# Performance work log

Hardware: AMD Instinct MI355X
Metric: run time of the kernel (lower is better)

## Reference

```python
import jax, jax.numpy as jnp
import numpy as np

# dims: S slots, B batch, D pred-rep dim, E slot-embedding dim, H hidden/output dim, V per-slot vocab
S, B, D, E, H, V = 7, 4096, 1024, 128, 512, 200
D0 = D + E  # layer-0 LSTM input size


def setup_inputs() -> dict:
    key = jax.random.key(0)
    ks = jax.random.split(key, 12)
    rn = lambda k, shape, s=0.02: jax.random.normal(k, shape, jnp.float32) * s
    return {
        "pred_reps": jax.random.normal(ks[0], (B, D), jnp.float32),
        "slot_labels": jax.random.randint(ks[1], (S, B), 0, V),
        "emb": rn(ks[2], (S, V, E), 1.0),
        # layer 0: per-slot LSTMCell + highway params
        "Wih0": rn(ks[3], (S, 4 * H, D0)), "Whh0": rn(ks[4], (S, 4 * H, H)),
        "bih0": jnp.zeros((S, 4 * H), jnp.float32), "bhh0": jnp.zeros((S, 4 * H), jnp.float32),
        "hwW0": rn(ks[5], (S, H, D0 + H)), "hwb0": jnp.zeros((S, H), jnp.float32),
        "linW0": rn(ks[6], (S, H, D0)),
        # layer 1 (input size = H)
        "Wih1": rn(ks[7], (S, 4 * H, H)), "Whh1": rn(ks[8], (S, 4 * H, H)),
        "bih1": jnp.zeros((S, 4 * H), jnp.float32), "bhh1": jnp.zeros((S, 4 * H), jnp.float32),
        "hwW1": rn(ks[9], (S, H, 2 * H)), "hwb1": jnp.zeros((S, H), jnp.float32),
        "linW1": rn(ks[10], (S, H, H)),
    }


def _lstm_cell(x, h, c, Wih, Whh, bih, bhh):
    # torch LSTMCell: gates ordered i, f, g, o
    gates = x @ Wih.T + bih + h @ Whh.T + bhh
    i, f, g, o = jnp.split(gates, 4, axis=-1)
    c_new = jax.nn.sigmoid(f) * c + jax.nn.sigmoid(i) * jnp.tanh(g)
    h_new = jax.nn.sigmoid(o) * jnp.tanh(c_new)
    return h_new, c_new


def reference(pred_reps, slot_labels, emb, Wih0, Whh0, bih0, bhh0, hwW0, hwb0, linW0,
              Wih1, Whh1, bih1, bhh1, hwW1, hwb1, linW1):
    def step(carry, xs):
        h0, c0, h1, c1 = carry
        (tbl, idx, wih0, whh0, bi0, bh0, hw0, hb0, lw0,
         wih1, whh1, bi1, bh1, hw1, hb1, lw1) = xs
        # per-slot embedding gather + concat with predicate reps  -> [B, D0]
        x = jnp.concatenate([pred_reps, tbl[idx]], axis=-1)
        # layer 0 cell + highway gate
        h0n, c0n = _lstm_cell(x, h0, c0, wih0, whh0, bi0, bh0)
        gate0 = jax.nn.sigmoid(jnp.concatenate([x, h0n], axis=-1) @ hw0.T + hb0)
        x1 = gate0 * h0n + (1.0 - gate0) * (x @ lw0.T)
        # layer 1 cell (its highway output is dead code in the original: curr_input
        # after the last layer is discarded, so we skip it -- same math)
        h1n, c1n = _lstm_cell(x1, h1, c1, wih1, whh1, bi1, bh1)
        return (h0n, c0n, h1n, c1n), None

    init = tuple(jnp.zeros((B, H), pred_reps.dtype) for _ in range(4))
    xs = (emb, slot_labels, Wih0, Whh0, bih0, bhh0, hwW0, hwb0, linW0,
          Wih1, Whh1, bih1, bhh1, hwW1, hwb1, linW1)
    carry, _ = jax.lax.scan(step, init, xs)
    return carry[2]  # last_h: top-layer hidden after final slot
```

## Files before the change

kernel.cpp:

```cpp
#include <hip/hip_runtime.h>
#include <stdint.h>

typedef unsigned short u16;

#define S_   7
#define B_   4096
#define D_   1024
#define E_   128
#define H_   512
#define V_   200
#define D0_  1152
#define K0_  1664
#define KX1  1024
#define G4H  2048
#define XW   2048
#define X1W  2048

typedef __bf16 bf16x8 __attribute__((ext_vector_type(8)));
typedef float  f32x4  __attribute__((ext_vector_type(4)));
typedef u16    u16x8  __attribute__((ext_vector_type(8)));

__device__ __forceinline__ u16 f2bf(float f) {
  union { float f; uint32_t u; } v; v.f = f;
  uint32_t r = v.u + 0x7fffu + ((v.u >> 16) & 1u);
  return (u16)(r >> 16);
}
__device__ __forceinline__ float bf2f(u16 b) {
  union { uint32_t u; float f; } v; v.u = ((uint32_t)b) << 16;
  return v.f;
}
__device__ __forceinline__ float sigmoidf_(float x) { return 1.0f / (1.0f + __expf(-x)); }
__device__ __forceinline__ float tanhf_(float x) {
  float t = __expf(-2.f * fabsf(x));
  return copysignf((1.f - t) / (1.f + t), x);
}

__device__ __forceinline__ void glds16(const u16* g, u16* l) {
  __builtin_amdgcn_global_load_lds(
      (const __attribute__((address_space(1))) uint32_t*)g,
      (__attribute__((address_space(3))) uint32_t*)l, 16, 0, 0);
}

__device__ __forceinline__ void cvt8s(const float* src, u16* dst) {
  const float4* p = (const float4*)src;
  float4 x = p[0], y = p[1];
  u16x8 o;
  o[0]=f2bf(x.x); o[1]=f2bf(x.y); o[2]=f2bf(x.z); o[3]=f2bf(x.w);
  o[4]=f2bf(y.x); o[5]=f2bf(y.y); o[6]=f2bf(y.z); o[7]=f2bf(y.w);
  *(u16x8*)dst = o;
}

template<int KK, int P1, int P2, int KA, int KB>
__global__ void pack_gw4(const float* __restrict__ Wih, const float* __restrict__ Whh,
                         u16* __restrict__ dst) {
  const int NG = KK / 8;
  const int stride = gridDim.x * 256;
  int idx = blockIdx.x * 256 + threadIdx.x;
  #pragma unroll
  for (int u = 0; u < 4; ++u) {
    int i = idx + u * stride;
    int sr = i / NG, kg = i - sr * NG;
    int k8 = kg * 8;
    long s = sr >> 11;
    int  r = sr & 2047;
    int  g = r >> 9, j = r & 511;
    long drow = (s << 11) + ((j >> 4) * 64 + g * 16 + (j & 15));
    const float* sp = (k8 < P1) ? Wih + (long)sr * KA + k8
                    : (k8 < P2) ? Whh + (long)sr * KB + (k8 - P1)
                                : Wih + (long)sr * KA + P1 + (k8 - P2);
    cvt8s(sp, &dst[drow * KK + k8]);
  }
}

template<int KS, bool Z2>
__global__ void pack_hw4(const float* __restrict__ src, u16* __restrict__ dst, int off16) {
  const int NG = K0_ / 8;
  const int stride = gridDim.x * 256;
  int idx = blockIdx.x * 256 + threadIdx.x;
  #pragma unroll
  for (int u = 0; u < 4; ++u) {
    int i = idx + u * stride;
    int sj = i / NG, kg = i - sj * NG;
    int k8 = kg * 8;
    long s = sj >> 9;
    int  j = sj & 511;
    long drow = (s << 10) + ((j >> 4) * 32 + off16 + (j & 15));
    u16* d = &dst[drow * K0_ + k8];
    if (Z2 && k8 >= 1024 && k8 < 1536) {
      u16x8 z = {};
      *(u16x8*)d = z;
    } else {
      const float* sp = (k8 < 1024) ? src + (long)sj * KS + k8
                      : (k8 < 1536) ? src + (long)sj * KS + 1152 + (k8 - 1024)
                                    : src + (long)sj * KS + 1024 + (k8 - 1536);
      cvt8s(sp, d);
    }
  }
}

__global__ void pack_predz4(const float* __restrict__ pred, u16* __restrict__ dst) {
  const int NG = XW / 8;
  const int stride = gridDim.x * 256;
  int idx = blockIdx.x * 256 + threadIdx.x;
  #pragma unroll
  for (int u = 0; u < 4; ++u) {
    int i = idx + u * stride;
    int row = i / NG, kg = i - row * NG;
    int k8 = kg * 8;
    u16* d = &dst[(long)row * XW + k8];
    if (k8 < 1024) {
      cvt8s(pred + (long)row * D_ + k8, d);
    } else {
      u16x8 z = {};
      *(u16x8*)d = z;
    }
  }
}

__global__ void xgather(const float* __restrict__ emb, const int* __restrict__ labels,
                        u16* __restrict__ EMB) {
  int b = blockIdx.x;
  int e = threadIdx.x;
  #pragma unroll
  for (int s = 0; s < S_; ++s) {
    int ix = labels[s * B_ + b];
    EMB[((long)(s * B_ + b)) * E_ + e] = f2bf(emb[((long)(s * V_ + ix)) * E_ + e]);
  }
}

__global__ void bias_sum(const float* __restrict__ a, const float* __restrict__ b,
                         float* __restrict__ o, int n) {
  int i = blockIdx.x * 256 + threadIdx.x;
  if (i < n) o[i] = a[i] + b[i];
}
__global__ void zero_f(float* __restrict__ p, int n) {
  for (int i = blockIdx.x * 256 + threadIdx.x; i < n; i += gridDim.x * 256) p[i] = 0.f;
}
__global__ void zero_u16k(u16* __restrict__ p, int n) {
  for (int i = blockIdx.x * 256 + threadIdx.x; i < n; i += gridDim.x * 256) p[i] = 0;
}

struct GemmP {
  const u16* r0; const u16* r1; const u16* r2;
  const u16* W;
  const float* bsum;
  float* cbuf;
  u16* hdst;
  float* hf32;
  const u16* h0src;
  int ld0, ld1, ld2, t1, t2, ldw, nt, ntn, cpx, hld, hoff, h0ld, mode;
};

__global__ __launch_bounds__(256)
void gemm_multi(GemmP pa, GemmP pb, GemmP pc, int nA, int nAB) {
  __shared__ __align__(16) u16 lds[4 * 8192];
  const int b = blockIdx.x;
  GemmP P = pc; int base = nAB;
  if (b < nAB) { P = pb; base = nA; }
  if (b < nA)  { P = pa; base = 0; }
  const int bidx = b - base;

  u16* lA = lds;
  u16* lW = lds + 2 * 8192;
  const int tid  = threadIdx.x;
  const int lane = tid & 63;
  const int wave = tid >> 6;
  const int bid  = (bidx & 7) * P.cpx + (bidx >> 3);
  const int tn = bid % P.ntn;
  const int tm = bid / P.ntn;
  const long row0 = (long)tm * 128;
  const long col0 = (long)tn * 128;
  const int wm = (wave >> 1) * 64;
  const int wn = (wave & 1) * 64;
  const int fr = lane & 15;
  const int fk = (lane >> 4) * 8;
  const int wr = wave * 32;

  const int srow = wr + (lane >> 3);
  const int scol = ((lane & 7) ^ ((lane >> 3) & 7)) * 8;
  const u16* gr0 = P.r0 + (row0 + srow) * (long)P.ld0 + scol;
  const u16* gr1 = P.r1 + (row0 + srow) * (long)P.ld1 + scol;
  const u16* gr2 = P.r2 + (row0 + srow) * (long)P.ld2 + scol;
  const u16* gw  = P.W  + (col0 + srow) * (long)P.ldw + scol;
  const int dst0 = wr * 64 + lane * 8;

  auto stage = [&](int t, int buf) {
    const u16* g; long ld;
    if (t < P.t1)      { g = gr0 + (long)t * 64;            ld = P.ld0; }
    else if (t < P.t2) { g = gr1 + (long)(t - P.t1) * 64;   ld = P.ld1; }
    else               { g = gr2 + (long)(t - P.t2) * 64;   ld = P.ld2; }
    const u16* gww = gw + (long)t * 64;
    u16* dA = lA + buf * 8192 + dst0;
    u16* dW = lW + buf * 8192 + dst0;
    #pragma unroll
    for (int i = 0; i < 4; ++i) {
      glds16(g   + (long)(i * 8) * ld,    dA + i * 512);
      glds16(gww + (long)(i * 8) * P.ldw, dW + i * 512);
    }
  };

  int aoff[4], woff[4];
  #pragma unroll
  for (int m = 0; m < 4; ++m) aoff[m] = (wm + m * 16 + fr) * 64;
  #pragma unroll
  for (int n = 0; n < 4; ++n) woff[n] = (wn + n * 16 + fr) * 64;
  const int swz = (fr & 7) << 3;
  const int kk0 = (0 + fk) ^ swz;
  const int kk1 = (32 + fk) ^ swz;

  f32x4 acc[4][4] = {};
  const int nt = P.nt;

  stage(0, 0);

  for (int t = 0; t < nt; ++t) {
    __syncthreads();
    if (t + 1 < nt) stage(t + 1, (t + 1) & 1);
    const u16* Ab = lA + (t & 1) * 8192;
    const u16* Wb = lW + (t & 1) * 8192;
    bf16x8 af0[4], wf0[4], af1[4], wf1[4];
    #pragma unroll
    for (int m = 0; m < 4; ++m) af0[m] = *(const bf16x8*)&Ab[aoff[m] + kk0];
    #pragma unroll
    for (int n = 0; n < 4; ++n) wf0[n] = *(const bf16x8*)&Wb[woff[n] + kk0];
    #pragma unroll
    for (int m = 0; m < 4; ++m) af1[m] = *(const bf16x8*)&Ab[aoff[m] + kk1];
    #pragma unroll
    for (int n = 0; n < 4; ++n) wf1[n] = *(const bf16x8*)&Wb[woff[n] + kk1];
    #pragma unroll
    for (int m = 0; m < 4; ++m)
      #pragma unroll
      for (int n = 0; n < 4; ++n)
        acc[m][n] = __builtin_amdgcn_mfma_f32_16x16x32_bf16(af0[m], wf0[n], acc[m][n], 0, 0, 0);
    #pragma unroll
    for (int m = 0; m < 4; ++m)
      #pragma unroll
      for (int n = 0; n < 4; ++n)
        acc[m][n] = __builtin_amdgcn_mfma_f32_16x16x32_bf16(af1[m], wf1[n], acc[m][n], 0, 0, 0);
  }

  const int cr = (lane >> 4) * 4;
  const int jg = wn >> 6;

  if (P.mode == 0) {
    const int j = tn * 32 + jg * 16 + fr;
    const float bi = P.bsum[j], bf = P.bsum[512 + j];
    const float bg = P.bsum[1024 + j], bo = P.bsum[1536 + j];
    #pragma unroll
    for (int m = 0; m < 4; ++m) {
      const long rbase = row0 + wm + m * 16 + cr;
      #pragma unroll
      for (int r = 0; r < 4; ++r) {
        const long ri = rbase + r;
        float gi = acc[m][0][r] + bi;
        float gf = acc[m][1][r] + bf;
        float gg = acc[m][2][r] + bg;
        float go = acc[m][3][r] + bo;
        float cv = P.cbuf[ri * H_ + j];
        float cn = sigmoidf_(gf) * cv + sigmoidf_(gi) * tanhf_(gg);
        float hn = sigmoidf_(go) * tanhf_(cn);
        P.cbuf[ri * H_ + j] = cn;
        P.hdst[ri * P.hld + P.hoff + j] = f2bf(hn);
        if (P.hf32) P.hf32[ri * H_ + j] = hn;
      }
    }
  } else {
    #pragma unroll
    for (int pp = 0; pp < 2; ++pp) {
      const int j = tn * 64 + jg * 32 + pp * 16 + fr;
      const float bj = P.bsum[j];
      #pragma unroll
      for (int m = 0; m < 4; ++m) {
        const long rbase = row0 + wm + m * 16 + cr;
        #pragma unroll
        for (int r = 0; r < 4; ++r) {
          const long ri = rbase + r;
          float gv = sigmoidf_(acc[m][2 * pp][r] + bj);
          float h0 = bf2f(P.h0src[ri * (long)P.h0ld + j]);
          float x1 = gv * h0 + (1.f - gv) * acc[m][2 * pp + 1][r];
          P.hdst[ri * P.hld + P.hoff + j] = f2bf(x1);
        }
      }
    }
  }
}

extern "C" void kernel_launch(void* const* d_in, const int* in_sizes, int n_in,
                              void* d_out, int out_size, void* d_ws, size_t ws_size,
                              hipStream_t stream) {
  const float* pred   = (const float*)d_in[0];
  const int*   labels = (const int*)d_in[1];
  const float* emb    = (const float*)d_in[2];
  const float* Wih0   = (const float*)d_in[3];
  const float* Whh0   = (const float*)d_in[4];
  const float* bih0   = (const float*)d_in[5];
  const float* bhh0   = (const float*)d_in[6];
  const float* hwW0   = (const float*)d_in[7];
  const float* hwb0   = (const float*)d_in[8];
  const float* linW0  = (const float*)d_in[9];
  const float* Wih1   = (const float*)d_in[10];
  const float* Whh1   = (const float*)d_in[11];
  const float* bih1   = (const float*)d_in[12];
  const float* bhh1   = (const float*)d_in[13];
  float* out = (float*)d_out;

  char* ws = (char*)d_ws;
  size_t off = 0;
  auto alloc = [&](size_t bytes) {
    char* p = ws + off;
    off = (off + bytes + 255) & ~(size_t)255;
    return p;
  };
  u16* WC0   = (u16*)alloc((size_t)S_ * G4H * K0_ * 2);
  u16* WHLw  = (u16*)alloc((size_t)S_ * 1024 * K0_ * 2);
  u16* WC1   = (u16*)alloc((size_t)S_ * G4H * KX1 * 2);
  u16* xcat  = (u16*)alloc((size_t)B_ * XW * 2);
  u16* EMB   = (u16*)alloc((size_t)S_ * B_ * E_ * 2);
  u16* x1cat = (u16*)alloc((size_t)B_ * X1W * 2);
  float* c0   = (float*)alloc((size_t)B_ * H_ * 4);
  float* c1   = (float*)alloc((size_t)B_ * H_ * 4);
  float* bs0  = (float*)alloc((size_t)S_ * G4H * 4);
  float* bs1  = (float*)alloc((size_t)S_ * G4H * 4);

  pack_gw4<K0_, 1024, 1536, D0_, H_><<<2912, 256, 0, stream>>>(Wih0, Whh0, WC0);
  pack_gw4<KX1,  512, 1024, H_,  H_><<<1792, 256, 0, stream>>>(Wih1, Whh1, WC1);
  pack_hw4<K0_, false><<<728, 256, 0, stream>>>(hwW0,  WHLw, 0);
  pack_hw4<D0_, true ><<<728, 256, 0, stream>>>(linW0, WHLw, 16);
  pack_predz4<<<1024, 256, 0, stream>>>(pred, xcat);
  xgather<<<B_, E_, 0, stream>>>(emb, labels, EMB);
  bias_sum<<<56, 256, 0, stream>>>(bih0, bhh0, bs0, S_ * G4H);
  bias_sum<<<56, 256, 0, stream>>>(bih1, bhh1, bs1, S_ * G4H);
  zero_f<<<256, 256, 0, stream>>>(c0, B_ * H_);
  zero_f<<<256, 256, 0, stream>>>(c1, B_ * H_);
  zero_u16k<<<512, 256, 0, stream>>>(x1cat, B_ * X1W);

  auto mkA = [&](int s) {
    GemmP P;
    P.r0 = xcat;                                 P.ld0 = XW;  P.t1 = 16;
    P.r1 = xcat + 1024 + ((s + 1) & 1) * 512;    P.ld1 = XW;  P.t2 = 24;
    P.r2 = EMB + (size_t)s * B_ * E_;            P.ld2 = E_;
    P.W = WC0 + (size_t)s * G4H * K0_;           P.ldw = K0_; P.nt = 26;
    P.ntn = 16; P.cpx = 64;
    P.bsum = bs0 + (size_t)s * G4H; P.cbuf = c0;
    P.hdst = xcat; P.hld = XW; P.hoff = 1024 + (s & 1) * 512;
    P.hf32 = nullptr; P.h0src = xcat; P.h0ld = 0; P.mode = 0;
    return P;
  };
  auto mkB = [&](int s) {
    GemmP P;
    P.r0 = xcat;                                 P.ld0 = XW;  P.t1 = 16;
    P.r1 = xcat + 1024 + (s & 1) * 512;          P.ld1 = XW;  P.t2 = 24;
    P.r2 = EMB + (size_t)s * B_ * E_;            P.ld2 = E_;
    P.W = WHLw + (size_t)s * 1024 * K0_;         P.ldw = K0_; P.nt = 26;
    P.ntn = 8; P.cpx = 32;
    P.bsum = hwb0 + (size_t)s * H_; P.cbuf = nullptr;
    P.hdst = x1cat; P.hld = X1W; P.hoff = (s & 1) * 512;
    P.hf32 = nullptr;
    P.h0src = xcat + 1024 + (s & 1) * 512; P.h0ld = XW; P.mode = 1;
    return P;
  };
  auto mkC = [&](int s) {
    GemmP P;
    P.r0 = x1cat + (s & 1) * 512;                P.ld0 = X1W; P.t1 = 8;
    P.r1 = x1cat + 1024 + ((s + 1) & 1) * 512;   P.ld1 = X1W; P.t2 = 16;
    P.r2 = P.r0;                                 P.ld2 = X1W;
    P.W = WC1 + (size_t)s * G4H * KX1;           P.ldw = KX1; P.nt = 16;
    P.ntn = 16; P.cpx = 64;
    P.bsum = bs1 + (size_t)s * G4H; P.cbuf = c1;
    P.hdst = x1cat; P.hld = X1W; P.hoff = 1024 + (s & 1) * 512;
    P.hf32 = (s == 6) ? out : nullptr; P.h0src = x1cat; P.h0ld = 0; P.mode = 0;
    return P;
  };

  for (int k = 0; k <= 8; ++k) {
    const int nA = (k <= 6) ? 512 : 0;
    const int nB = (k >= 1 && k <= 7) ? 256 : 0;
    const int nC = (k >= 2) ? 512 : 0;
    GemmP pa, pb, pc;
    if (nA) pa = mkA(k);
    if (nB) pb = mkB(k - 1);
    if (nC) pc = mkC(k - 2);
    GemmP any = nA ? pa : (nB ? pb : pc);
    if (!nA) pa = any;
    if (!nB) pb = any;
    if (!nC) pc = any;
    gemm_multi<<<nA + nB + nC, 256, 0, stream>>>(pa, pb, pc, nA, nA + nB);
  }
}
```

Measured before the change: 660.0 us.

## Fold per-slot weight packing into GEMM launches and halve K-tile depth

Weight packing now runs one slot at a time as extra blocks appended to the wavefront GEMM launches, so slot k+1's packing overlaps slot k's GEMMs instead of a separate upfront pass. The GEMM K tile shrinks from 64 to 32, halving LDS to 32KB. Launch bounds now target 4 blocks per CU, and the tile-to-XCD mapping uses shift parameters. The trade-offs are twice as many K iterations and barriers, possible register pressure from the occupancy hint, and packing blocks competing with GEMM blocks for CUs.

```diff
diff --git a/kernel.cpp b/kernel.cpp
--- a/kernel.cpp
+++ b/kernel.cpp
@@ -50,49 +50,41 @@
   *(u16x8*)dst = o;
 }
 
-template<int KK, int P1, int P2, int KA, int KB>
-__global__ void pack_gw4(const float* __restrict__ Wih, const float* __restrict__ Whh,
-                         u16* __restrict__ dst) {
-  const int NG = KK / 8;
-  const int stride = gridDim.x * 256;
-  int idx = blockIdx.x * 256 + threadIdx.x;
+__device__ __forceinline__ void pk_gates(const float* __restrict__ Wih,
+                                         const float* __restrict__ Whh,
+                                         u16* __restrict__ dst,
+                                         int idx, int stride, int NG, int KK,
+                                         int P1, int P2, int KA, int KB) {
   #pragma unroll
   for (int u = 0; u < 4; ++u) {
     int i = idx + u * stride;
-    int sr = i / NG, kg = i - sr * NG;
+    int r = i / NG, kg = i - r * NG;
     int k8 = kg * 8;
-    long s = sr >> 11;
-    int  r = sr & 2047;
-    int  g = r >> 9, j = r & 511;
-    long drow = (s << 11) + ((j >> 4) * 64 + g * 16 + (j & 15));
-    const float* sp = (k8 < P1) ? Wih + (long)sr * KA + k8
-                    : (k8 < P2) ? Whh + (long)sr * KB + (k8 - P1)
-                                : Wih + (long)sr * KA + P1 + (k8 - P2);
+    int g = r >> 9, j = r & 511;
+    long drow = (j >> 4) * 64 + g * 16 + (j & 15);
+    const float* sp = (k8 < P1) ? Wih + (long)r * KA + k8
+                    : (k8 < P2) ? Whh + (long)r * KB + (k8 - P1)
+                                : Wih + (long)r * KA + P1 + (k8 - P2);
     cvt8s(sp, &dst[drow * KK + k8]);
   }
 }
-
-template<int KS, bool Z2>
-__global__ void pack_hw4(const float* __restrict__ src, u16* __restrict__ dst, int off16) {
-  const int NG = K0_ / 8;
-  const int stride = gridDim.x * 256;
-  int idx = blockIdx.x * 256 + threadIdx.x;
+__device__ __forceinline__ void pk_hw(const float* __restrict__ src,
+                                      u16* __restrict__ dst,
+                                      int idx, int stride, int off16, int KS, bool Z2) {
   #pragma unroll
   for (int u = 0; u < 4; ++u) {
     int i = idx + u * stride;
-    int sj = i / NG, kg = i - sj * NG;
+    int r = i / 208, kg = i - r * 208;
     int k8 = kg * 8;
-    long s = sj >> 9;
-    int  j = sj & 511;
-    long drow = (s << 10) + ((j >> 4) * 32 + off16 + (j & 15));
+    long drow = ((r & 511) >> 4) * 32 + off16 + (r & 15);
     u16* d = &dst[drow * K0_ + k8];
     if (Z2 && k8 >= 1024 && k8 < 1536) {
       u16x8 z = {};
       *(u16x8*)d = z;
     } else {
-      const float* sp = (k8 < 1024) ? src + (long)sj * KS + k8
-                      : (k8 < 1536) ? src + (long)sj * KS + 1152 + (k8 - 1024)
-                                    : src + (long)sj * KS + 1024 + (k8 - 1536);
+      const float* sp = (k8 < 1024) ? src + (long)r * KS + k8
+                      : (k8 < 1536) ? src + (long)r * KS + 1152 + (k8 - 1024)
+                                    : src + (long)r * KS + 1024 + (k8 - 1536);
       cvt8s(sp, d);
     }
   }
@@ -141,72 +133,88 @@
 }
 
 struct GemmP {
-  const u16* r0; const u16* r1; const u16* r2;
-  const u16* W;
-  const float* bsum;
-  float* cbuf;
-  u16* hdst;
-  float* hf32;
-  const u16* h0src;
-  int ld0, ld1, ld2, t1, t2, ldw, nt, ntn, cpx, hld, hoff, h0ld, mode;
+  const u16 *r0, *r1, *r2, *W;
+  const float *bsum;
+  float *cbuf;
+  u16 *hdst;
+  float *hf32;
+  const u16 *h0src;
+  int ld0, ld1, ld2, t1, t2, ldw, nt, ntn, tnw_sh, ncc_sh, tmw, hld, hoff, h0ld, mode;
 };
-
-__global__ __launch_bounds__(256)
-void gemm_multi(GemmP pa, GemmP pb, GemmP pc, int nA, int nAB) {
-  __shared__ __align__(16) u16 lds[4 * 8192];
-  const int b = blockIdx.x;
+struct PackP {
+  const float *wih0, *whh0, *wih1, *whh1, *hww, *linw;
+  u16 *wc0, *wc1, *whl;
+};
+
+__global__ __launch_bounds__(256, 4)
+void gemm_multi(GemmP pa, GemmP pb, GemmP pc, PackP pk, int nA, int nAB, int nABC) {
+  const int b   = blockIdx.x;
+  const int tid = threadIdx.x;
+
+  if (b >= nABC) {
+    int rb = b - nABC;
+    if (rb < 416) {
+      pk_gates(pk.wih0, pk.whh0, pk.wc0, rb * 256 + tid, 416 * 256,
+               208, K0_, 1024, 1536, D0_, H_);
+    } else if (rb < 672) {
+      pk_gates(pk.wih1, pk.whh1, pk.wc1, (rb - 416) * 256 + tid, 256 * 256,
+               128, KX1, 512, 1024, H_, H_);
+    } else {
+      int sb = rb - 672;
+      if (sb < 104) pk_hw(pk.hww,  pk.whl, sb * 256 + tid,        104 * 256, 0,  K0_, false);
+      else          pk_hw(pk.linw, pk.whl, (sb - 104) * 256 + tid, 104 * 256, 16, D0_, true);
+    }
+    return;
+  }
+
+  __shared__ __align__(16) u16 lds[4 * 4096];
   GemmP P = pc; int base = nAB;
   if (b < nAB) { P = pb; base = nA; }
   if (b < nA)  { P = pa; base = 0; }
   const int bidx = b - base;
 
   u16* lA = lds;
-  u16* lW = lds + 2 * 8192;
-  const int tid  = threadIdx.x;
+  u16* lW = lds + 2 * 4096;
   const int lane = tid & 63;
   const int wave = tid >> 6;
-  const int bid  = (bidx & 7) * P.cpx + (bidx >> 3);
-  const int tn = bid % P.ntn;
-  const int tm = bid / P.ntn;
+  const int xcd = bidx & 7, ci = bidx >> 3;
+  const int tn = ((xcd & ((1 << P.ncc_sh) - 1)) << P.tnw_sh) | (ci & ((1 << P.tnw_sh) - 1));
+  const int tm = (xcd >> P.ncc_sh) * P.tmw + (ci >> P.tnw_sh);
   const long row0 = (long)tm * 128;
   const long col0 = (long)tn * 128;
   const int wm = (wave >> 1) * 64;
   const int wn = (wave & 1) * 64;
   const int fr = lane & 15;
-  const int fk = (lane >> 4) * 8;
-  const int wr = wave * 32;
-
-  const int srow = wr + (lane >> 3);
-  const int scol = ((lane & 7) ^ ((lane >> 3) & 7)) * 8;
-  const u16* gr0 = P.r0 + (row0 + srow) * (long)P.ld0 + scol;
-  const u16* gr1 = P.r1 + (row0 + srow) * (long)P.ld1 + scol;
-  const u16* gr2 = P.r2 + (row0 + srow) * (long)P.ld2 + scol;
-  const u16* gw  = P.W  + (col0 + srow) * (long)P.ldw + scol;
-  const int dst0 = wr * 64 + lane * 8;
+  const int hi = lane >> 4;
+
+  const int s_row = wave * 16 + (lane >> 2);
+  const int scol = ((lane & 3) ^ ((lane >> 3) & 3)) * 8;
+  const u16* gr0 = P.r0 + (row0 + s_row) * (long)P.ld0 + scol;
+  const u16* gr1 = P.r1 + (row0 + s_row) * (long)P.ld1 + scol;
+  const u16* gr2 = P.r2 + (row0 + s_row) * (long)P.ld2 + scol;
+  const u16* gw  = P.W  + (col0 + s_row) * (long)P.ldw + scol;
+  const int dst0 = wave * 512 + lane * 8;
 
   auto stage = [&](int t, int buf) {
     const u16* g; long ld;
-    if (t < P.t1)      { g = gr0 + (long)t * 64;            ld = P.ld0; }
-    else if (t < P.t2) { g = gr1 + (long)(t - P.t1) * 64;   ld = P.ld1; }
-    else               { g = gr2 + (long)(t - P.t2) * 64;   ld = P.ld2; }
-    const u16* gww = gw + (long)t * 64;
-    u16* dA = lA + buf * 8192 + dst0;
-    u16* dW = lW + buf * 8192 + dst0;
-    #pragma unroll
-    for (int i = 0; i < 4; ++i) {
-      glds16(g   + (long)(i * 8) * ld,    dA + i * 512);
-      glds16(gww + (long)(i * 8) * P.ldw, dW + i * 512);
-    }
-  };
-
+    if (t < P.t1)      { g = gr0 + (long)t * 32;          ld = P.ld0; }
+    else if (t < P.t2) { g = gr1 + (long)(t - P.t1) * 32; ld = P.ld1; }
+    else               { g = gr2 + (long)(t - P.t2) * 32; ld = P.ld2; }
+    const u16* gww = gw + (long)t * 32;
+    u16* dA = lA + buf * 4096 + dst0;
+    u16* dW = lW + buf * 4096 + dst0;
+    glds16(g,           dA);
+    glds16(g + 64 * ld, dA + 2048);
+    glds16(gww,                      dW);
+    glds16(gww + 64 * (long)P.ldw,   dW + 2048);
+  };
+
+  const int koff = (hi ^ ((fr >> 1) & 3)) * 8;
   int aoff[4], woff[4];
   #pragma unroll
-  for (int m = 0; m < 4; ++m) aoff[m] = (wm + m * 16 + fr) * 64;
-  #pragma unroll
-  for (int n = 0; n < 4; ++n) woff[n] = (wn + n * 16 + fr) * 64;
-  const int swz = (fr & 7) << 3;
-  const int kk0 = (0 + fk) ^ swz;
-  const int kk1 = (32 + fk) ^ swz;
+  for (int m = 0; m < 4; ++m) aoff[m] = (wm + m * 16 + fr) * 32 + koff;
+  #pragma unroll
+  for (int n = 0; n < 4; ++n) woff[n] = (wn + n * 16 + fr) * 32 + koff;
 
   f32x4 acc[4][4] = {};
   const int nt = P.nt;
@@ -216,27 +224,18 @@
   for (int t = 0; t < nt; ++t) {
     __syncthreads();
     if (t + 1 < nt) stage(t + 1, (t + 1) & 1);
-    const u16* Ab = lA + (t & 1) * 8192;
-    const u16* Wb = lW + (t & 1) * 8192;
-    bf16x8 af0[4], wf0[4], af1[4], wf1[4];
+    const u16* Ab = lA + (t & 1) * 4096;
+    const u16* Wb = lW + (t & 1) * 4096;
+    bf16x8 af[4], wf[4];
     #pragma unroll
-    for (int m = 0; m < 4; ++m) af0[m] = *(const bf16x8*)&Ab[aoff[m] + kk0];
+    for (int m = 0; m < 4; ++m) af[m] = *(const bf16x8*)&Ab[aoff[m]];
     #pragma unroll
-    for (int n = 0; n < 4; ++n) wf0[n] = *(const bf16x8*)&Wb[woff[n] + kk0];
-    #pragma unroll
-    for (int m = 0; m < 4; ++m) af1[m] = *(const bf16x8*)&Ab[aoff[m] + kk1];
-    #pragma unroll
-    for (int n = 0; n < 4; ++n) wf1[n] = *(const bf16x8*)&Wb[woff[n] + kk1];
+    for (int n = 0; n < 4; ++n) wf[n] = *(const bf16x8*)&Wb[woff[n]];
     #pragma unroll
     for (int m = 0; m < 4; ++m)
       #pragma unroll
       for (int n = 0; n < 4; ++n)
-        acc[m][n] = __builtin_amdgcn_mfma_f32_16x16x32_bf16(af0[m], wf0[n], acc[m][n], 0, 0, 0);
-    #pragma unroll
-    for (int m = 0; m < 4; ++m)
-      #pragma unroll
-      for (int n = 0; n < 4; ++n)
-        acc[m][n] = __builtin_amdgcn_mfma_f32_16x16x32_bf16(af1[m], wf1[n], acc[m][n], 0, 0, 0);
+        acc[m][n] = __builtin_amdgcn_mfma_f32_16x16x32_bf16(af[m], wf[n], acc[m][n], 0, 0, 0);
   }
 
   const int cr = (lane >> 4) * 4;
@@ -322,25 +321,37 @@
   float* bs0  = (float*)alloc((size_t)S_ * G4H * 4);
   float* bs1  = (float*)alloc((size_t)S_ * G4H * 4);
 
-  pack_gw4<K0_, 1024, 1536, D0_, H_><<<2912, 256, 0, stream>>>(Wih0, Whh0, WC0);
-  pack_gw4<KX1,  512, 1024, H_,  H_><<<1792, 256, 0, stream>>>(Wih1, Whh1, WC1);
-  pack_hw4<K0_, false><<<728, 256, 0, stream>>>(hwW0,  WHLw, 0);
-  pack_hw4<D0_, true ><<<728, 256, 0, stream>>>(linW0, WHLw, 16);
+  auto mkPk = [&](int s) {
+    PackP K;
+    K.wih0 = Wih0 + (size_t)s * G4H * D0_;
+    K.whh0 = Whh0 + (size_t)s * G4H * H_;
+    K.wih1 = Wih1 + (size_t)s * G4H * H_;
+    K.whh1 = Whh1 + (size_t)s * G4H * H_;
+    K.hww  = hwW0 + (size_t)s * H_ * K0_;
+    K.linw = linW0 + (size_t)s * H_ * D0_;
+    K.wc0  = WC0  + (size_t)s * G4H * K0_;
+    K.wc1  = WC1  + (size_t)s * G4H * KX1;
+    K.whl  = WHLw + (size_t)s * 1024 * K0_;
+    return K;
+  };
+
+  GemmP z = {};
+  gemm_multi<<<880, 256, 0, stream>>>(z, z, z, mkPk(0), 0, 0, 0);
   pack_predz4<<<1024, 256, 0, stream>>>(pred, xcat);
   xgather<<<B_, E_, 0, stream>>>(emb, labels, EMB);
   bias_sum<<<56, 256, 0, stream>>>(bih0, bhh0, bs0, S_ * G4H);
   bias_sum<<<56, 256, 0, stream>>>(bih1, bhh1, bs1, S_ * G4H);
   zero_f<<<256, 256, 0, stream>>>(c0, B_ * H_);
   zero_f<<<256, 256, 0, stream>>>(c1, B_ * H_);
-  zero_u16k<<<512, 256, 0, stream>>>(x1cat, B_ * X1W);
+  zero_u16k<<<2048, 256, 0, stream>>>(x1cat, B_ * X1W);
 
   auto mkA = [&](int s) {
     GemmP P;
-    P.r0 = xcat;                                 P.ld0 = XW;  P.t1 = 16;
-    P.r1 = xcat + 1024 + ((s + 1) & 1) * 512;    P.ld1 = XW;  P.t2 = 24;
-    P.r2 = EMB + (size_t)s * B_ * E_;            P.ld2 = E_;
-    P.W = WC0 + (size_t)s * G4H * K0_;           P.ldw = K0_; P.nt = 26;
-    P.ntn = 16; P.cpx = 64;
+    P.r0 = xcat;                               P.ld0 = XW;  P.t1 = 32;
+    P.r1 = xcat + 1024 + ((s + 1) & 1) * 512;  P.ld1 = XW;  P.t2 = 48;
+    P.r2 = EMB + (size_t)s * B_ * E_;          P.ld2 = E_;
+    P.W = WC0 + (size_t)s * G4H * K0_;         P.ldw = K0_; P.nt = 52;
+    P.ntn = 16; P.tnw_sh = 3; P.ncc_sh = 1; P.tmw = 8;
     P.bsum = bs0 + (size_t)s * G4H; P.cbuf = c0;
     P.hdst = xcat; P.hld = XW; P.hoff = 1024 + (s & 1) * 512;
     P.hf32 = nullptr; P.h0src = xcat; P.h0ld = 0; P.mode = 0;
@@ -348,11 +359,11 @@
   };
   auto mkB = [&](int s) {
     GemmP P;
-    P.r0 = xcat;                                 P.ld0 = XW;  P.t1 = 16;
-    P.r1 = xcat + 1024 + (s & 1) * 512;          P.ld1 = XW;  P.t2 = 24;
-    P.r2 = EMB + (size_t)s * B_ * E_;            P.ld2 = E_;
-    P.W = WHLw + (size_t)s * 1024 * K0_;         P.ldw = K0_; P.nt = 26;
-    P.ntn = 8; P.cpx = 32;
+    P.r0 = xcat;                               P.ld0 = XW;  P.t1 = 32;
+    P.r1 = xcat + 1024 + (s & 1) * 512;        P.ld1 = XW;  P.t2 = 48;
+    P.r2 = EMB + (size_t)s * B_ * E_;          P.ld2 = E_;
+    P.W = WHLw + (size_t)s * 1024 * K0_;       P.ldw = K0_; P.nt = 52;
+    P.ntn = 8; P.tnw_sh = 2; P.ncc_sh = 1; P.tmw = 8;
     P.bsum = hwb0 + (size_t)s * H_; P.cbuf = nullptr;
     P.hdst = x1cat; P.hld = X1W; P.hoff = (s & 1) * 512;
     P.hf32 = nullptr;
@@ -361,11 +372,11 @@
   };
   auto mkC = [&](int s) {
     GemmP P;
-    P.r0 = x1cat + (s & 1) * 512;                P.ld0 = X1W; P.t1 = 8;
-    P.r1 = x1cat + 1024 + ((s + 1) & 1) * 512;   P.ld1 = X1W; P.t2 = 16;
-    P.r2 = P.r0;                                 P.ld2 = X1W;
-    P.W = WC1 + (size_t)s * G4H * KX1;           P.ldw = KX1; P.nt = 16;
-    P.ntn = 16; P.cpx = 64;
+    P.r0 = x1cat + (s & 1) * 512;              P.ld0 = X1W; P.t1 = 16;
+    P.r1 = x1cat + 1024 + ((s + 1) & 1) * 512; P.ld1 = X1W; P.t2 = 32;
+    P.r2 = P.r0;                               P.ld2 = X1W;
+    P.W = WC1 + (size_t)s * G4H * KX1;         P.ldw = KX1; P.nt = 32;
+    P.ntn = 16; P.tnw_sh = 3; P.ncc_sh = 1; P.tmw = 8;
     P.bsum = bs1 + (size_t)s * G4H; P.cbuf = c1;
     P.hdst = x1cat; P.hld = X1W; P.hoff = 1024 + (s & 1) * 512;
     P.hf32 = (s == 6) ? out : nullptr; P.h0src = x1cat; P.h0ld = 0; P.mode = 0;
@@ -376,6 +387,7 @@
     const int nA = (k <= 6) ? 512 : 0;
     const int nB = (k >= 1 && k <= 7) ? 256 : 0;
     const int nC = (k >= 2) ? 512 : 0;
+    const int nD = (k <= 5) ? 880 : 0;
     GemmP pa, pb, pc;
     if (nA) pa = mkA(k);
     if (nB) pb = mkB(k - 1);
@@ -384,6 +396,8 @@
     if (!nA) pa = any;
     if (!nB) pb = any;
     if (!nC) pc = any;
-    gemm_multi<<<nA + nB + nC, 256, 0, stream>>>(pa, pb, pc, nA, nA + nB);
-  }
-}
+    PackP pk = mkPk(nD ? (k + 1) : 0);
+    gemm_multi<<<nA + nB + nC + nD, 256, 0, stream>>>(pa, pb, pc, pk,
+                                                      nA, nA + nB, nA + nB + nC);
+  }
+}
```

Result: no change. 657.2 us (-0.4%).
